# Kernel tuning notes

Measured on AMD Instinct MI355X. Metric: run time of the kernel, lower is better.

The kernel has to match this reference:

```python
import jax, jax.numpy as jnp
import numpy as np

N_NODES = 50000
N_EDGES = 800000
F_IN, D1, N_CLS = 128, 128, 64


def gcn_conv(x, W, b, src, dst, n):
    # x: [N, Fin] -> linear transform then normalized scatter-add aggregation
    h = x @ W  # [N, Fout]
    deg = jnp.zeros((n,), h.dtype).at[dst].add(jnp.ones((dst.shape[0],), h.dtype))
    dis = jnp.where(deg > 0, jax.lax.rsqrt(jnp.maximum(deg, 1.0)), 0.0)  # deg^-1/2, inf->0
    norm = dis[src] * dis[dst]  # [E_tot]
    msgs = norm[:, None] * h[src]  # gather source features, scale by sym norm
    out = jax.ops.segment_sum(msgs, dst, num_segments=n)  # scatter-add to targets
    return out + b


def setup_inputs() -> dict:
    key = jax.random.key(0)
    ks = jax.random.split(key, 6)
    x = jax.random.normal(ks[0], (N_NODES, F_IN), dtype=jnp.float32)
    edge_index = jax.random.randint(ks[1], (2, N_EDGES), 0, N_NODES, dtype=jnp.int64)
    W1 = jax.random.normal(ks[2], (F_IN, D1), dtype=jnp.float32) / np.sqrt(F_IN)
    b1 = jnp.zeros((D1,), dtype=jnp.float32)
    W2 = jax.random.normal(ks[3], (D1, N_CLS), dtype=jnp.float32) / np.sqrt(D1)
    b2 = jnp.zeros((N_CLS,), dtype=jnp.float32)
    return {"x": x, "edge_index": edge_index, "W1": W1, "b1": b1, "W2": W2, "b2": b2}


def reference(x, edge_index, W1, b1, W2, b2):
    n = x.shape[0]
    loops = jnp.arange(n, dtype=edge_index.dtype)
    src = jnp.concatenate([edge_index[0], loops])  # add self-loops (PyG default)
    dst = jnp.concatenate([edge_index[1], loops])
    h = gcn_conv(x, W1, b1, src, dst, n)
    h = jax.nn.relu(h)
    # F.dropout(training=self.training) is identity in eval mode
    out = gcn_conv(h, W2, b2, src, dst, n)
    return out
```

## Files before the change

### kernel.cpp

```cpp
#include <hip/hip_runtime.h>

#define NN 50000
#define NE 800000
#define CAP 64
#define SLICE 6250

typedef unsigned int   u32;
typedef unsigned short u16;

__device__ inline u16 f2bf(float f) {
    u32 u = __float_as_uint(f);
    u32 r = (u + 0x7FFF + ((u >> 16) & 1)) >> 16;
    return (u16)r;
}
__device__ inline float bf_lo(u32 u) { return __uint_as_float(u << 16); }
__device__ inline float bf_hi(u32 u) { return __uint_as_float(u & 0xFFFF0000u); }


__global__ __launch_bounds__(256) void build_ell(const int* __restrict__ ei,
                                                 int* __restrict__ cnt,
                                                 u16* __restrict__ ell) {
    const int s  = blockIdx.x & 7;
    const int g  = blockIdx.x >> 3;
    const int ng = gridDim.x >> 3;
    const int lo = s * SLICE, hi = lo + SLICE;
    for (int e0 = (g * 256 + (int)threadIdx.x) * 4; e0 < NE; e0 += ng * 1024) {
        int4 d4 = *(const int4*)(ei + NE + e0);
        int dv[4] = {d4.x, d4.y, d4.z, d4.w};
#pragma unroll
        for (int k = 0; k < 4; ++k) {
            int d = dv[k];
            if (d >= lo && d < hi) {
                int src = ei[e0 + k];
                int pos = atomicAdd(&cnt[d], 1);
                if (pos < CAP) ell[d * CAP + pos] = (u16)src;
            }
        }
    }
}

__global__ __launch_bounds__(256) void calc_dis(const int* __restrict__ cnt,
                                                float* __restrict__ dis) {
    int i = blockIdx.x * 256 + threadIdx.x;
    if (i >= NN) return;
    dis[i] = rsqrtf((float)(cnt[i] + 1));
}


template <int NOUT>
__global__ __launch_bounds__(256) void gemm_k128(const float* __restrict__ A,
                                                 const float* __restrict__ W,
                                                 u16* __restrict__ C, int M) {
    constexpr int CT = NOUT / 16;
    __shared__ float Al[8][132];
    __shared__ float Wl[8][NOUT + 4];

    const int tid  = threadIdx.x;
    const int tcol = tid & 15;
    const int trow = tid >> 4;
    const int row0 = blockIdx.x * 128;

    float acc[8][CT];
#pragma unroll
    for (int i = 0; i < 8; ++i)
#pragma unroll
        for (int j = 0; j < CT; ++j) acc[i][j] = 0.0f;

    const int lrow = tid >> 1;
    const int lk4  = (tid & 1) * 4;
    const bool rv  = (row0 + lrow) < M;
    const float* arow = A + (size_t)(row0 + lrow) * 128;

    constexpr int W4 = 8 * NOUT / 4;
    const int wkrow = tid / (NOUT / 4);
    const int wc4   = (tid % (NOUT / 4)) * 4;

    for (int kt = 0; kt < 128; kt += 8) {
        float4 av = rv ? *(const float4*)(arow + kt + lk4)
                       : make_float4(0.f, 0.f, 0.f, 0.f);
        Al[lk4 + 0][lrow] = av.x;
        Al[lk4 + 1][lrow] = av.y;
        Al[lk4 + 2][lrow] = av.z;
        Al[lk4 + 3][lrow] = av.w;
        if (tid < W4) {
            *(float4*)&Wl[wkrow][wc4] =
                *(const float4*)(W + (size_t)(kt + wkrow) * NOUT + wc4);
        }
        __syncthreads();
#pragma unroll
        for (int k = 0; k < 8; ++k) {
            float4 a0 = *(const float4*)&Al[k][trow * 4];
            float4 a1 = *(const float4*)&Al[k][trow * 4 + 64];
            float a[8] = {a0.x, a0.y, a0.z, a0.w, a1.x, a1.y, a1.z, a1.w};
            float4 b0 = *(const float4*)&Wl[k][tcol * 4];
            if constexpr (CT == 8) {
                float4 b1 = *(const float4*)&Wl[k][tcol * 4 + 64];
                float b[8] = {b0.x, b0.y, b0.z, b0.w, b1.x, b1.y, b1.z, b1.w};
#pragma unroll
                for (int i = 0; i < 8; ++i)
#pragma unroll
                    for (int j = 0; j < 8; ++j) acc[i][j] += a[i] * b[j];
            } else {
                float b[4] = {b0.x, b0.y, b0.z, b0.w};
#pragma unroll
                for (int i = 0; i < 8; ++i)
#pragma unroll
                    for (int j = 0; j < 4; ++j) acc[i][j] += a[i] * b[j];
            }
        }
        __syncthreads();
    }

#pragma unroll
    for (int i = 0; i < 8; ++i) {
        int row = row0 + trow * 4 + ((i < 4) ? i : (64 + i - 4));
        if (row < M) {
            *(ushort4*)&C[(size_t)row * NOUT + tcol * 4] =
                make_ushort4(f2bf(acc[i][0]), f2bf(acc[i][1]),
                             f2bf(acc[i][2]), f2bf(acc[i][3]));
            if constexpr (CT == 8) {
                *(ushort4*)&C[(size_t)row * NOUT + tcol * 4 + 64] =
                    make_ushort4(f2bf(acc[i][4]), f2bf(acc[i][5]),
                                 f2bf(acc[i][6]), f2bf(acc[i][7]));
            }
        }
    }
}


template <int F, bool RELU>
__global__ __launch_bounds__(256) void aggregate(const u16* __restrict__ H,
                                                 const u16* __restrict__ ell,
                                                 const int* __restrict__ cnt,
                                                 const float* __restrict__ dis,
                                                 const float* __restrict__ bias,
                                                 float* __restrict__ out) {
    int node = (int)((blockIdx.x * 256 + threadIdx.x) >> 6);
    int lane = threadIdx.x & 63;
    if (node >= NN) return;

    int ne = min(cnt[node], CAP);
    float di = dis[node];
    int   s_l  = (lane < ne) ? (int)ell[node * CAP + lane] : 0;
    float ds_l = (lane < ne) ? dis[s_l] * di : 0.0f;

    if constexpr (F == 128) {
        float ax = 0.f, ay = 0.f;
        int j = 0;
        for (; j + 8 <= ne; j += 8) {
            u32 v[8]; float n[8];
#pragma unroll
            for (int t = 0; t < 8; ++t) {
                int s = __shfl(s_l, j + t);
                n[t] = __shfl(ds_l, j + t);
                v[t] = ((const u32*)(H + (size_t)s * 128))[lane];
            }
#pragma unroll
            for (int t = 0; t < 8; ++t) {
                ax += n[t] * bf_lo(v[t]);
                ay += n[t] * bf_hi(v[t]);
            }
        }
        for (; j < ne; ++j) {
            int s = __shfl(s_l, j);
            float n = __shfl(ds_l, j);
            u32 v = ((const u32*)(H + (size_t)s * 128))[lane];
            ax += n * bf_lo(v);
            ay += n * bf_hi(v);
        }
        u32 vs = ((const u32*)(H + (size_t)node * 128))[lane];
        ax += di * di * bf_lo(vs);
        ay += di * di * bf_hi(vs);
        ax += bias[lane * 2]; ay += bias[lane * 2 + 1];
        if (RELU) { ax = fmaxf(ax, 0.f); ay = fmaxf(ay, 0.f); }
        *(float2*)(out + (size_t)node * 128 + lane * 2) = make_float2(ax, ay);
    } else {
        float a = 0.f;
        int j = 0;
        for (; j + 8 <= ne; j += 8) {
            u16 v[8]; float n[8];
#pragma unroll
            for (int t = 0; t < 8; ++t) {
                int s = __shfl(s_l, j + t);
                n[t] = __shfl(ds_l, j + t);
                v[t] = H[(size_t)s * 64 + lane];
            }
#pragma unroll
            for (int t = 0; t < 8; ++t)
                a += n[t] * __uint_as_float((u32)v[t] << 16);
        }
        for (; j < ne; ++j) {
            int s = __shfl(s_l, j);
            float n = __shfl(ds_l, j);
            a += n * __uint_as_float((u32)H[(size_t)s * 64 + lane] << 16);
        }
        a += di * di * __uint_as_float((u32)H[(size_t)node * 64 + lane] << 16);
        a += bias[lane];
        if (RELU) a = fmaxf(a, 0.f);
        out[(size_t)node * 64 + lane] = a;
    }
}


extern "C" void kernel_launch(void* const* d_in, const int* in_sizes, int n_in,
                              void* d_out, int out_size, void* d_ws, size_t ws_size,
                              hipStream_t stream) {
    const float* x  = (const float*)d_in[0];
    const int*   ei = (const int*)d_in[1];
    const float* W1 = (const float*)d_in[2];
    const float* b1 = (const float*)d_in[3];
    const float* W2 = (const float*)d_in[4];
    const float* b2 = (const float*)d_in[5];
    float* out = (float*)d_out;

    char* ws = (char*)d_ws;
    const size_t NPAD = 50176;
    int*   cnt  = (int*)ws;
    float* dis  = (float*)(ws + NPAD * 4);
    u16*   ell  = (u16*)(ws + 2 * NPAD * 4);
    u16*   Hbf  = (u16*)(ws + 2 * NPAD * 4 + (size_t)NN * CAP * 2);
    float* bufB = (float*)(ws + 2 * NPAD * 4 + (size_t)NN * CAP * 2
                              + (size_t)NN * 128 * 2);

    hipMemsetAsync(cnt, 0, NN * sizeof(int), stream);
    build_ell<<<1600, 256, 0, stream>>>(ei, cnt, ell);
    calc_dis<<<(NN + 255) / 256, 256, 0, stream>>>(cnt, dis);

    gemm_k128<128><<<(NN + 127) / 128, 256, 0, stream>>>(x, W1, Hbf, NN);
    aggregate<128, true><<<(NN + 3) / 4, 256, 0, stream>>>(Hbf, ell, cnt, dis, b1, bufB);

    gemm_k128<64><<<(NN + 127) / 128, 256, 0, stream>>>(bufB, W2, Hbf, NN);
    aggregate<64, false><<<(NN + 3) / 4, 256, 0, stream>>>(Hbf, ell, cnt, dis, b2, out);
}
```

Baseline: 239.6 us.

## Use split-bf16 MFMA GEMMs and restructure aggregation with vectorized row gathers

Replaces the FP32 SIMT GEMMs with MFMA bf16 GEMMs that split each operand into high and low bf16 parts, using three MFMAs to approximate FP32 accuracy. The weights are pre-split and pre-swizzled by a new prep kernel. The aggregation kernel now has lane groups each gather a whole row with 16-byte loads, folds the self-loop in as an extra neighbour, and combines partial sums with cross-lane shuffles. The degree-normalisation kernel is removed and rsqrt is computed inline. This trades extra MFMA work and shuffle reductions for fewer FP32 FMAs and wider, more coalesced gathers, and it changes the neighbour cap from 64 to 63.

```diff
diff --git a/kernel.cpp b/kernel.cpp
--- a/kernel.cpp
+++ b/kernel.cpp
@@ -7,12 +7,14 @@
 
 typedef unsigned int   u32;
 typedef unsigned short u16;
+typedef __attribute__((ext_vector_type(8))) short short8;
+typedef __attribute__((ext_vector_type(4))) float f32x4;
 
 __device__ inline u16 f2bf(float f) {
     u32 u = __float_as_uint(f);
-    u32 r = (u + 0x7FFF + ((u >> 16) & 1)) >> 16;
-    return (u16)r;
-}
+    return (u16)((u + 0x7FFF + ((u >> 16) & 1)) >> 16);
+}
+__device__ inline float bfval(u16 h) { return __uint_as_float(((u32)h) << 16); }
 __device__ inline float bf_lo(u32 u) { return __uint_as_float(u << 16); }
 __device__ inline float bf_hi(u32 u) { return __uint_as_float(u & 0xFFFF0000u); }
 
@@ -39,92 +41,72 @@
     }
 }
 
-__global__ __launch_bounds__(256) void calc_dis(const int* __restrict__ cnt,
-                                                float* __restrict__ dis) {
+
+__global__ __launch_bounds__(256) void prep_w(const float* __restrict__ W1,
+                                              const float* __restrict__ W2,
+                                              u16* __restrict__ W1h, u16* __restrict__ W1l,
+                                              u16* __restrict__ W2h, u16* __restrict__ W2l) {
     int i = blockIdx.x * 256 + threadIdx.x;
-    if (i >= NN) return;
-    dis[i] = rsqrtf((float)(cnt[i] + 1));
+    const float* W; u16 *Dh, *Dl; int NOUT, idx;
+    if (i < 16384) { W = W1; Dh = W1h; Dl = W1l; NOUT = 128; idx = i; }
+    else           { idx = i - 16384; if (idx >= 8192) return;
+                     W = W2; Dh = W2h; Dl = W2l; NOUT = 64; }
+    int j = idx & 7, l = (idx >> 3) & 63, kc = (idx >> 9) & 3, t = idx >> 11;
+    int k = kc * 32 + (l >> 4) * 8 + j;
+    int n = t * 16 + (l & 15);
+    float w = W[k * NOUT + n];
+    u16 h = f2bf(w);
+    Dh[idx] = h;
+    Dl[idx] = f2bf(w - bfval(h));
 }
 
 
 template <int NOUT>
-__global__ __launch_bounds__(256) void gemm_k128(const float* __restrict__ A,
-                                                 const float* __restrict__ W,
+__global__ __launch_bounds__(256) void gemm_mfma(const float* __restrict__ A,
+                                                 const u16* __restrict__ Wh,
+                                                 const u16* __restrict__ Wl,
                                                  u16* __restrict__ C, int M) {
-    constexpr int CT = NOUT / 16;
-    __shared__ float Al[8][132];
-    __shared__ float Wl[8][NOUT + 4];
-
-    const int tid  = threadIdx.x;
-    const int tcol = tid & 15;
-    const int trow = tid >> 4;
-    const int row0 = blockIdx.x * 128;
-
-    float acc[8][CT];
-#pragma unroll
-    for (int i = 0; i < 8; ++i)
-#pragma unroll
-        for (int j = 0; j < CT; ++j) acc[i][j] = 0.0f;
-
-    const int lrow = tid >> 1;
-    const int lk4  = (tid & 1) * 4;
-    const bool rv  = (row0 + lrow) < M;
-    const float* arow = A + (size_t)(row0 + lrow) * 128;
-
-    constexpr int W4 = 8 * NOUT / 4;
-    const int wkrow = tid / (NOUT / 4);
-    const int wc4   = (tid % (NOUT / 4)) * 4;
-
-    for (int kt = 0; kt < 128; kt += 8) {
-        float4 av = rv ? *(const float4*)(arow + kt + lk4)
-                       : make_float4(0.f, 0.f, 0.f, 0.f);
-        Al[lk4 + 0][lrow] = av.x;
-        Al[lk4 + 1][lrow] = av.y;
-        Al[lk4 + 2][lrow] = av.z;
-        Al[lk4 + 3][lrow] = av.w;
-        if (tid < W4) {
-            *(float4*)&Wl[wkrow][wc4] =
-                *(const float4*)(W + (size_t)(kt + wkrow) * NOUT + wc4);
-        }
-        __syncthreads();
-#pragma unroll
-        for (int k = 0; k < 8; ++k) {
-            float4 a0 = *(const float4*)&Al[k][trow * 4];
-            float4 a1 = *(const float4*)&Al[k][trow * 4 + 64];
-            float a[8] = {a0.x, a0.y, a0.z, a0.w, a1.x, a1.y, a1.z, a1.w};
-            float4 b0 = *(const float4*)&Wl[k][tcol * 4];
-            if constexpr (CT == 8) {
-                float4 b1 = *(const float4*)&Wl[k][tcol * 4 + 64];
-                float b[8] = {b0.x, b0.y, b0.z, b0.w, b1.x, b1.y, b1.z, b1.w};
-#pragma unroll
-                for (int i = 0; i < 8; ++i)
-#pragma unroll
-                    for (int j = 0; j < 8; ++j) acc[i][j] += a[i] * b[j];
-            } else {
-                float b[4] = {b0.x, b0.y, b0.z, b0.w};
-#pragma unroll
-                for (int i = 0; i < 8; ++i)
-#pragma unroll
-                    for (int j = 0; j < 4; ++j) acc[i][j] += a[i] * b[j];
-            }
-        }
-        __syncthreads();
-    }
-
-#pragma unroll
-    for (int i = 0; i < 8; ++i) {
-        int row = row0 + trow * 4 + ((i < 4) ? i : (64 + i - 4));
-        if (row < M) {
-            *(ushort4*)&C[(size_t)row * NOUT + tcol * 4] =
-                make_ushort4(f2bf(acc[i][0]), f2bf(acc[i][1]),
-                             f2bf(acc[i][2]), f2bf(acc[i][3]));
-            if constexpr (CT == 8) {
-                *(ushort4*)&C[(size_t)row * NOUT + tcol * 4 + 64] =
-                    make_ushort4(f2bf(acc[i][4]), f2bf(acc[i][5]),
-                                 f2bf(acc[i][6]), f2bf(acc[i][7]));
-            }
-        }
-    }
+    constexpr int NT = NOUT / 16;
+    const int tid = threadIdx.x;
+    const int w = tid >> 6, l = tid & 63;
+    const int m = l & 15, q = l >> 4;
+
+    int arow = blockIdx.x * 64 + w * 16 + m;
+    const float* Ar = A + (size_t)min(arow, M - 1) * 128;
+
+    f32x4 acc[NT] = {};
+
+#pragma unroll
+    for (int kc = 0; kc < 4; ++kc) {
+        float p[8];
+        *(float4*)&p[0] = *(const float4*)(Ar + kc * 32 + q * 8);
+        *(float4*)&p[4] = *(const float4*)(Ar + kc * 32 + q * 8 + 4);
+        short8 ah, al;
+#pragma unroll
+        for (int j = 0; j < 8; ++j) {
+            u16 h = f2bf(p[j]);
+            ah[j] = (short)h;
+            al[j] = (short)f2bf(p[j] - bfval(h));
+        }
+#pragma unroll
+        for (int t = 0; t < NT; ++t) {
+            size_t bo = ((size_t)(t * 4 + kc) * 64 + l) * 8;
+            short8 bh = *(const short8*)(Wh + bo);
+            short8 bl = *(const short8*)(Wl + bo);
+            acc[t] = __builtin_amdgcn_mfma_f32_16x16x32_bf16(ah, bh, acc[t], 0, 0, 0);
+            acc[t] = __builtin_amdgcn_mfma_f32_16x16x32_bf16(al, bh, acc[t], 0, 0, 0);
+            acc[t] = __builtin_amdgcn_mfma_f32_16x16x32_bf16(ah, bl, acc[t], 0, 0, 0);
+        }
+    }
+
+    int growbase = blockIdx.x * 64 + w * 16 + q * 4;
+#pragma unroll
+    for (int t = 0; t < NT; ++t)
+#pragma unroll
+        for (int r = 0; r < 4; ++r) {
+            int grow = growbase + r;
+            if (grow < M) C[(size_t)grow * NOUT + t * 16 + m] = f2bf(acc[t][r]);
+        }
 }
 
 
@@ -132,72 +114,74 @@
 __global__ __launch_bounds__(256) void aggregate(const u16* __restrict__ H,
                                                  const u16* __restrict__ ell,
                                                  const int* __restrict__ cnt,
-                                                 const float* __restrict__ dis,
                                                  const float* __restrict__ bias,
                                                  float* __restrict__ out) {
-    int node = (int)((blockIdx.x * 256 + threadIdx.x) >> 6);
-    int lane = threadIdx.x & 63;
+    const int tid = threadIdx.x;
+    const int node = (int)((blockIdx.x * 256 + tid) >> 6);
     if (node >= NN) return;
-
-    int ne = min(cnt[node], CAP);
-    float di = dis[node];
-    int   s_l  = (lane < ne) ? (int)ell[node * CAP + lane] : 0;
-    float ds_l = (lane < ne) ? dis[s_l] * di : 0.0f;
-
-    if constexpr (F == 128) {
-        float ax = 0.f, ay = 0.f;
-        int j = 0;
-        for (; j + 8 <= ne; j += 8) {
-            u32 v[8]; float n[8];
-#pragma unroll
-            for (int t = 0; t < 8; ++t) {
-                int s = __shfl(s_l, j + t);
-                n[t] = __shfl(ds_l, j + t);
-                v[t] = ((const u32*)(H + (size_t)s * 128))[lane];
-            }
-#pragma unroll
-            for (int t = 0; t < 8; ++t) {
-                ax += n[t] * bf_lo(v[t]);
-                ay += n[t] * bf_hi(v[t]);
-            }
-        }
-        for (; j < ne; ++j) {
-            int s = __shfl(s_l, j);
-            float n = __shfl(ds_l, j);
-            u32 v = ((const u32*)(H + (size_t)s * 128))[lane];
-            ax += n * bf_lo(v);
-            ay += n * bf_hi(v);
-        }
-        u32 vs = ((const u32*)(H + (size_t)node * 128))[lane];
-        ax += di * di * bf_lo(vs);
-        ay += di * di * bf_hi(vs);
-        ax += bias[lane * 2]; ay += bias[lane * 2 + 1];
-        if (RELU) { ax = fmaxf(ax, 0.f); ay = fmaxf(ay, 0.f); }
-        *(float2*)(out + (size_t)node * 128 + lane * 2) = make_float2(ax, ay);
+    const int lane = tid & 63;
+
+    const int cn = cnt[node];
+    const int ne = min(cn, 63);
+    const float di = rsqrtf((float)(cn + 1));
+    int   s_l = (lane < ne) ? (int)ell[(size_t)node * CAP + lane] : node;
+    float n_l = (lane <= ne) ? rsqrtf((float)(cnt[s_l] + 1)) * di : 0.0f;
+
+    constexpr int G = (F == 128) ? 4 : 8;
+    constexpr int L = 64 / G;
+    const int g = lane / L;
+    const int ci = lane & (L - 1);
+
+    const int m = ne + 1;
+    const int mPad = (m + 2 * G - 1) & ~(2 * G - 1);
+
+    float acc[8] = {0, 0, 0, 0, 0, 0, 0, 0};
+    for (int j = 0; j < mPad; j += 2 * G) {
+        int   sA = __shfl(s_l, j + g);
+        float nA = __shfl(n_l, j + g);
+        int   sB = __shfl(s_l, j + G + g);
+        float nB = __shfl(n_l, j + G + g);
+        uint4 vA = *(const uint4*)(H + (size_t)sA * F + ci * 8);
+        uint4 vB = *(const uint4*)(H + (size_t)sB * F + ci * 8);
+        acc[0] += nA * bf_lo(vA.x); acc[1] += nA * bf_hi(vA.x);
+        acc[2] += nA * bf_lo(vA.y); acc[3] += nA * bf_hi(vA.y);
+        acc[4] += nA * bf_lo(vA.z); acc[5] += nA * bf_hi(vA.z);
+        acc[6] += nA * bf_lo(vA.w); acc[7] += nA * bf_hi(vA.w);
+        acc[0] += nB * bf_lo(vB.x); acc[1] += nB * bf_hi(vB.x);
+        acc[2] += nB * bf_lo(vB.y); acc[3] += nB * bf_hi(vB.y);
+        acc[4] += nB * bf_lo(vB.z); acc[5] += nB * bf_hi(vB.z);
+        acc[6] += nB * bf_lo(vB.w); acc[7] += nB * bf_hi(vB.w);
+    }
+
+#pragma unroll
+    for (int i = 0; i < 8; ++i) {
+        if (F == 64) acc[i] += __shfl_xor(acc[i], 8);
+        acc[i] += __shfl_xor(acc[i], 16);
+        acc[i] += __shfl_xor(acc[i], 32);
+    }
+
+    if (F == 128) {
+        if (lane < 32) {
+            int part = lane >> 4;
+            int c0 = (lane & 15) * 8 + part * 4;
+            float4 b4 = *(const float4*)(bias + c0);
+            float4 o = make_float4(acc[part * 4 + 0] + b4.x, acc[part * 4 + 1] + b4.y,
+                                   acc[part * 4 + 2] + b4.z, acc[part * 4 + 3] + b4.w);
+            if (RELU) { o.x = fmaxf(o.x, 0.f); o.y = fmaxf(o.y, 0.f);
+                        o.z = fmaxf(o.z, 0.f); o.w = fmaxf(o.w, 0.f); }
+            *(float4*)(out + (size_t)node * 128 + c0) = o;
+        }
     } else {
-        float a = 0.f;
-        int j = 0;
-        for (; j + 8 <= ne; j += 8) {
-            u16 v[8]; float n[8];
-#pragma unroll
-            for (int t = 0; t < 8; ++t) {
-                int s = __shfl(s_l, j + t);
-                n[t] = __shfl(ds_l, j + t);
-                v[t] = H[(size_t)s * 64 + lane];
-            }
-#pragma unroll
-            for (int t = 0; t < 8; ++t)
-                a += n[t] * __uint_as_float((u32)v[t] << 16);
-        }
-        for (; j < ne; ++j) {
-            int s = __shfl(s_l, j);
-            float n = __shfl(ds_l, j);
-            a += n * __uint_as_float((u32)H[(size_t)s * 64 + lane] << 16);
-        }
-        a += di * di * __uint_as_float((u32)H[(size_t)node * 64 + lane] << 16);
-        a += bias[lane];
-        if (RELU) a = fmaxf(a, 0.f);
-        out[(size_t)node * 64 + lane] = a;
+        if (lane < 16) {
+            int part = (lane >> 3) & 1;
+            int c0 = (lane & 7) * 8 + part * 4;
+            float4 b4 = *(const float4*)(bias + c0);
+            float4 o = make_float4(acc[part * 4 + 0] + b4.x, acc[part * 4 + 1] + b4.y,
+                                   acc[part * 4 + 2] + b4.z, acc[part * 4 + 3] + b4.w);
+            if (RELU) { o.x = fmaxf(o.x, 0.f); o.y = fmaxf(o.y, 0.f);
+                        o.z = fmaxf(o.z, 0.f); o.w = fmaxf(o.w, 0.f); }
+            *(float4*)(out + (size_t)node * 64 + c0) = o;
+        }
     }
 }
 
@@ -214,21 +198,25 @@
     float* out = (float*)d_out;
 
     char* ws = (char*)d_ws;
-    const size_t NPAD = 50176;
-    int*   cnt  = (int*)ws;
-    float* dis  = (float*)(ws + NPAD * 4);
-    u16*   ell  = (u16*)(ws + 2 * NPAD * 4);
-    u16*   Hbf  = (u16*)(ws + 2 * NPAD * 4 + (size_t)NN * CAP * 2);
-    float* bufB = (float*)(ws + 2 * NPAD * 4 + (size_t)NN * CAP * 2
-                              + (size_t)NN * 128 * 2);
+    size_t off = 0;
+    int* cnt = (int*)ws;                     off += (size_t)51200 * 4;
+    u16* ell = (u16*)(ws + off);             off += (size_t)NN * CAP * 2;
+    off = (off + 255) & ~(size_t)255;
+    u16* W1h = (u16*)(ws + off);             off += 16384 * 2;
+    u16* W1l = (u16*)(ws + off);             off += 16384 * 2;
+    u16* W2h = (u16*)(ws + off);             off += 8192 * 2;
+    u16* W2l = (u16*)(ws + off);             off += 8192 * 2;
+    off = (off + 255) & ~(size_t)255;
+    u16* Hbf = (u16*)(ws + off);             off += (size_t)NN * 128 * 2;
+    float* bufB = (float*)(ws + off);        off += (size_t)NN * 128 * 4;
 
     hipMemsetAsync(cnt, 0, NN * sizeof(int), stream);
+    prep_w<<<96, 256, 0, stream>>>(W1, W2, W1h, W1l, W2h, W2l);
     build_ell<<<1600, 256, 0, stream>>>(ei, cnt, ell);
-    calc_dis<<<(NN + 255) / 256, 256, 0, stream>>>(cnt, dis);
-
-    gemm_k128<128><<<(NN + 127) / 128, 256, 0, stream>>>(x, W1, Hbf, NN);
-    aggregate<128, true><<<(NN + 3) / 4, 256, 0, stream>>>(Hbf, ell, cnt, dis, b1, bufB);
-
-    gemm_k128<64><<<(NN + 127) / 128, 256, 0, stream>>>(bufB, W2, Hbf, NN);
-    aggregate<64, false><<<(NN + 3) / 4, 256, 0, stream>>>(Hbf, ell, cnt, dis, b2, out);
-}
+
+    gemm_mfma<128><<<(NN + 63) / 64, 256, 0, stream>>>(x, W1h, W1l, Hbf, NN);
+    aggregate<128, true><<<(NN + 3) / 4, 256, 0, stream>>>(Hbf, ell, cnt, b1, bufB);
+
+    gemm_mfma<64><<<(NN + 63) / 64, 256, 0, stream>>>(bufB, W2h, W2l, Hbf, NN);
+    aggregate<64, false><<<(NN + 3) / 4, 256, 0, stream>>>(Hbf, ell, cnt, b2, out);
+}
```

Measured after the change: 202.7 us. 15.4% less time.
